# Performance work log

Measured on AMD Instinct MI355X. Metric: run time of the kernel, lower is better.

The kernel has to match this reference:

```python
import jax, jax.numpy as jnp
import numpy as np

N_NODES = 100000


def setup_inputs() -> dict:
    key = jax.random.key(0)
    k1, k2, k3 = jax.random.split(key, 3)
    x = jax.random.normal(k1, (N_NODES, 256), dtype=jnp.float32)
    edge_index = jax.random.randint(k2, (2, 1600000), 0, N_NODES, dtype=jnp.int64)
    W = jax.random.normal(k3, (256, 128), dtype=jnp.float32) * (1.0 / np.sqrt(256.0))
    b = jnp.zeros((128,), dtype=jnp.float32)
    alpha = jnp.full((128,), 0.25, dtype=jnp.float32)  # PReLU default init
    return {"x": x, "edge_index": edge_index, "W": W, "b": b, "alpha": alpha}


def reference(x, edge_index, W, b, alpha):
    N = x.shape[0]
    # --- GCNConv: add self-loops ---
    loops = jnp.arange(N, dtype=edge_index.dtype)
    row = jnp.concatenate([edge_index[0], loops])  # source nodes
    col = jnp.concatenate([edge_index[1], loops])  # destination nodes
    # symmetric normalization: deg computed at destinations (self-loops => deg >= 1)
    deg = jax.ops.segment_sum(jnp.ones(col.shape, x.dtype), col, num_segments=N)
    dinv = jax.lax.rsqrt(deg)
    norm = dinv[row] * dinv[col]  # [E+N]
    # linear transform then normalized scatter-add aggregation
    h = x @ W  # [N, H]
    msg = h[row] * norm[:, None]  # [E+N, H]
    out = jax.ops.segment_sum(msg, col, num_segments=N) + b  # bias after aggregation
    # --- PReLU (per-channel) ---
    return jnp.where(out >= 0, out, alpha * out)
```

## Files before the change

kernel.cpp:

```cpp
#include <hip/hip_runtime.h>

constexpr int KDIM  = 256;
constexpr int HDIM  = 128;
constexpr int BK    = 128;
constexpr int CHUNK = 8192;
constexpr int NBMAX = 800;

typedef __bf16 bf16x8 __attribute__((ext_vector_type(8)));
typedef float  f32x4  __attribute__((ext_vector_type(4)));

__device__ __forceinline__ ushort f2bf(float f) {
    unsigned u = __float_as_uint(f);
    unsigned r = (u + 0x7fffu + ((u >> 16) & 1u)) >> 16;
    return (ushort)r;
}

__device__ __forceinline__ void acc8i(float* a, uint2 u, float s) {
    int x = (int)u.x, y = (int)u.y;
    a[0] += s * (float)((x << 24) >> 24);
    a[1] += s * (float)((x << 16) >> 24);
    a[2] += s * (float)((x <<  8) >> 24);
    a[3] += s * (float)( x        >> 24);
    a[4] += s * (float)((y << 24) >> 24);
    a[5] += s * (float)((y << 16) >> 24);
    a[6] += s * (float)((y <<  8) >> 24);
    a[7] += s * (float)( y        >> 24);
}

__global__ __launch_bounds__(512) void prep_sort_kernel(
    const float* __restrict__ W, ushort* __restrict__ Wt, char* __restrict__ hsb8,
    float* __restrict__ hscale,
    const int* __restrict__ row, const int* __restrict__ col,
    uint* __restrict__ ebuf, int* __restrict__ histG, int* __restrict__ localOff,
    int n, int e, int nbv, int gblk) {
    __shared__ uint dst[CHUNK];
    __shared__ int hist[NBMAX], excl[NBMAX], cur[NBMAX];
    __shared__ int ws2[8];
    int b = blockIdx.x, t = threadIdx.x;
    if (b < 8) {
        int g = b * 512 + t;
        int lane = g & 63, cn = g >> 6;
        int c = cn >> 3, nf = cn & 7;
        int ncol = nf * 16 + (lane & 15);
        int k0 = c * 32 + (lane >> 4) * 8;
        ushort* dp = Wt + (size_t)g * 8;
        #pragma unroll
        for (int j = 0; j < 8; ++j) dp[j] = f2bf(W[(k0 + j) * HDIM + ncol]);
        return;
    }
    if (b == 8) {
        if (t < 32) ((uint*)(hsb8 + (size_t)n * HDIM))[t] = 0;
        if (t == 32) hscale[n] = 0.f;
        return;
    }
    int g = b - 9;
    int lane = t & 63, w = t >> 6;
    for (int i = t; i < nbv; i += 512) hist[i] = 0;
    __syncthreads();
    int lo = g * CHUNK, hi = min(lo + CHUNK, e);
    int colr[16];
    #pragma unroll
    for (int k = 0; k < 4; ++k) {
        int i0 = lo + (k * 512 + t) * 4;
        if (i0 + 3 < hi) {
            int4 c4 = *(const int4*)(col + i0);
            colr[k * 4 + 0] = c4.x; colr[k * 4 + 1] = c4.y;
            colr[k * 4 + 2] = c4.z; colr[k * 4 + 3] = c4.w;
            atomicAdd(&hist[c4.x >> 7], 1); atomicAdd(&hist[c4.y >> 7], 1);
            atomicAdd(&hist[c4.z >> 7], 1); atomicAdd(&hist[c4.w >> 7], 1);
        } else {
            #pragma unroll
            for (int j = 0; j < 4; ++j) {
                int i = i0 + j;
                int c = (i < hi) ? col[i] : -1;
                colr[k * 4 + j] = c;
                if (c >= 0) atomicAdd(&hist[c >> 7], 1);
            }
        }
    }
    __syncthreads();
    {
        int b0 = t * 2;
        int h0 = (b0 < nbv) ? hist[b0] : 0;
        int h1 = (b0 + 1 < nbv) ? hist[b0 + 1] : 0;
        int s = h0 + h1, incl = s;
        #pragma unroll
        for (int d = 1; d < 64; d <<= 1) { int u = __shfl_up(incl, d, 64); if (lane >= d) incl += u; }
        if (lane == 63) ws2[w] = incl;
        __syncthreads();
        int add = 0;
        #pragma unroll
        for (int i = 0; i < 8; ++i) if (i < w) add += ws2[i];
        int run = add + incl - s;
        if (b0 < nbv)     { excl[b0] = run;          cur[b0] = run; }
        if (b0 + 1 < nbv) { excl[b0 + 1] = run + h0; cur[b0 + 1] = run + h0; }
    }
    __syncthreads();
    #pragma unroll
    for (int k = 0; k < 4; ++k) {
        int i0 = lo + (k * 512 + t) * 4;
        if (i0 + 3 < hi) {
            int4 r4 = *(const int4*)(row + i0);
            int rr[4] = {r4.x, r4.y, r4.z, r4.w};
            #pragma unroll
            for (int j = 0; j < 4; ++j) {
                int c = colr[k * 4 + j];
                int p = atomicAdd(&cur[c >> 7], 1);
                dst[p] = ((uint)rr[j] << 7) | (uint)(c & 127);
            }
        } else {
            #pragma unroll
            for (int j = 0; j < 4; ++j) {
                int i = i0 + j, c = colr[k * 4 + j];
                if (c >= 0) {
                    int p = atomicAdd(&cur[c >> 7], 1);
                    dst[p] = ((uint)row[i] << 7) | (uint)(c & 127);
                }
            }
        }
    }
    __syncthreads();
    int cnt = hi - lo;
    for (int k = 0; k < 4; ++k) {
        int i0 = (k * 512 + t) * 4;
        if (i0 + 3 < cnt) *(uint4*)(ebuf + lo + i0) = *(uint4*)&dst[i0];
        else for (int j = 0; j < 4; ++j) if (i0 + j < cnt) ebuf[lo + i0 + j] = dst[i0 + j];
    }
    for (int i = t; i < nbv; i += 512) {
        histG[i * gblk + g]    = hist[i];
        localOff[i * gblk + g] = excl[i];
    }
}

__global__ __launch_bounds__(256) void scanA_kernel(const int* __restrict__ in,
                                                    int* __restrict__ partial, int n) {
    int t = threadIdx.x, base = blockIdx.x * 1024;
    int s = 0;
    #pragma unroll
    for (int j = 0; j < 4; ++j) {
        int i = base + j * 256 + t;
        if (i < n) s += in[i];
    }
    __shared__ int ws[4];
    #pragma unroll
    for (int d = 1; d < 64; d <<= 1) s += __shfl_xor(s, d, 64);
    int lane = t & 63, w = t >> 6;
    if (lane == 0) ws[w] = s;
    __syncthreads();
    if (t == 0) partial[blockIdx.x] = ws[0] + ws[1] + ws[2] + ws[3];
}

__global__ void scanB_kernel(int* __restrict__ partial, int nb) {
    int t = threadIdx.x;
    int v = (t < nb) ? partial[t] : 0;
    int orig = v;
    int lane = t & 63, w = t >> 6;
    #pragma unroll
    for (int d = 1; d < 64; d <<= 1) { int u = __shfl_up(v, d, 64); if (lane >= d) v += u; }
    __shared__ int ws[4];
    if (lane == 63) ws[w] = v;
    __syncthreads();
    int add = 0;
    #pragma unroll
    for (int i = 0; i < 4; ++i) if (i < w) add += ws[i];
    if (t < nb) partial[t] = v + add - orig;
}

__global__ __launch_bounds__(256) void scanC_kernel(const int* __restrict__ in,
                                                    const int* __restrict__ partial,
                                                    int* __restrict__ out, int n) {
    int t = threadIdx.x, base = blockIdx.x * 1024;
    int vals[4], tsum = 0;
    #pragma unroll
    for (int j = 0; j < 4; ++j) {
        int i = base + t * 4 + j;
        vals[j] = (i < n) ? in[i] : 0;
        tsum += vals[j];
    }
    int lane = t & 63, w = t >> 6;
    int incl = tsum;
    #pragma unroll
    for (int d = 1; d < 64; d <<= 1) { int u = __shfl_up(incl, d, 64); if (lane >= d) incl += u; }
    __shared__ int ws[4];
    if (lane == 63) ws[w] = incl;
    __syncthreads();
    int add = partial[blockIdx.x];
    #pragma unroll
    for (int i = 0; i < 4; ++i) if (i < w) add += ws[i];
    int run = add + incl - tsum;
    #pragma unroll
    for (int j = 0; j < 4; ++j) {
        int i = base + t * 4 + j;
        if (i < n) out[i] = run;
        run += vals[j];
    }
}

__global__ __launch_bounds__(256) void fine_kernel(const uint* __restrict__ ebuf,
                                                   const int* __restrict__ histG,
                                                   const int* __restrict__ localOff,
                                                   const int* __restrict__ histS,
                                                   uint* __restrict__ csr,
                                                   int* __restrict__ deg,
                                                   int* __restrict__ offs,
                                                   float* __restrict__ dinv,
                                                   int e, int nbv, int gblk, int n) {
    __shared__ uint elist[4096];
    __shared__ uint csrl[4096];
    __shared__ int hist[BK], excl[BK], cur[BK];
    int b = blockIdx.x, t = threadIdx.x;
    int seg0 = histS[b * gblk];
    int seg1 = (b + 1 < nbv) ? histS[(b + 1) * gblk] : e;
    int cnt = min(seg1 - seg0, 4096);

    if (t < BK) { hist[t] = 0; cur[t] = 0; }
    for (int g = t; g < gblk; g += 256) {
        int c   = histG[b * gblk + g];
        int src = g * CHUNK + localOff[b * gblk + g];
        int dst = histS[b * gblk + g] - seg0;
        for (int i = 0; i < c; ++i) elist[dst + i] = ebuf[src + i];
    }
    __syncthreads();
    for (int i = t; i < cnt; i += 256) atomicAdd(&hist[elist[i] & 127], 1);
    __syncthreads();
    if (t < 64) {
        int v0 = hist[2 * t], v1 = hist[2 * t + 1];
        int s = v0 + v1, incl = s;
        #pragma unroll
        for (int d = 1; d < 64; d <<= 1) { int u = __shfl_up(incl, d, 64); if (t >= d) incl += u; }
        int base = incl - s;
        excl[2 * t] = base; excl[2 * t + 1] = base + v0;
    }
    __syncthreads();
    for (int i = t; i < cnt; i += 256) {
        uint v = elist[i];
        int d = v & 127;
        int r = atomicAdd(&cur[d], 1);
        csrl[excl[d] + r] = v >> 7;
    }
    __syncthreads();
    for (int i = t; i < cnt; i += 256) csr[seg0 + i] = csrl[i];
    if (t < BK) {
        int node = b * BK + t;
        if (node < n) {
            int dg = hist[t];
            deg[node]  = dg;
            offs[node] = seg0 + excl[t];
            dinv[node] = rsqrtf((float)(dg + 1));
        }
    }
}


constexpr int MT = 64;
constexpr int XS_STRIDE = 264;

__global__ __launch_bounds__(256) void gemm_kernel(const float* __restrict__ x,
                                                   const ushort* __restrict__ Wt,
                                                   const float* __restrict__ dinv,
                                                   char* __restrict__ hsb8,
                                                   float* __restrict__ hscale, int n) {
    __shared__ ushort xs[MT * XS_STRIDE];
    __shared__ float sdinv[MT];
    __shared__ uint rmaxs[16];
    int t = threadIdx.x, lane = t & 63, w = t >> 6;
    int row0 = blockIdx.x * MT;

    bf16x8 bfrag[8][2];
    #pragma unroll
    for (int c = 0; c < 8; ++c)
        #pragma unroll
        for (int f = 0; f < 2; ++f)
            bfrag[c][f] = *(const bf16x8*)(Wt + (size_t)(((c * 8) + (w * 2 + f)) * 64 + lane) * 8);

    #pragma unroll
    for (int i = 0; i < 16; ++i) {
        int rl = w * 16 + i;
        int gr = row0 + rl; if (gr >= n) gr = n - 1;
        float4 v = *(const float4*)(x + (size_t)gr * KDIM + lane * 4);
        ushort4 o;
        o.x = f2bf(v.x); o.y = f2bf(v.y); o.z = f2bf(v.z); o.w = f2bf(v.w);
        *(ushort4*)(xs + rl * XS_STRIDE + lane * 4) = o;
    }
    if (t < MT) { int g = row0 + t; sdinv[t] = dinv[(g < n) ? g : (n - 1)]; }
    __syncthreads();

    for (int s = 0; s < MT / 16; ++s) {
        f32x4 acc0 = {0.f, 0.f, 0.f, 0.f}, acc1 = {0.f, 0.f, 0.f, 0.f};
        #pragma unroll
        for (int c = 0; c < 8; ++c) {
            const ushort* ap = xs + (s * 16 + (lane & 15)) * XS_STRIDE + c * 32 + (lane >> 4) * 8;
            bf16x8 afrag = *(const bf16x8*)ap;
            acc0 = __builtin_amdgcn_mfma_f32_16x16x32_bf16(afrag, bfrag[c][0], acc0, 0, 0, 0);
            acc1 = __builtin_amdgcn_mfma_f32_16x16x32_bf16(afrag, bfrag[c][1], acc1, 0, 0, 0);
        }
        if (t < 16) rmaxs[t] = 0;
        __syncthreads();
        float v0[4], v1[4];
        #pragma unroll
        for (int reg = 0; reg < 4; ++reg) {
            int rl = s * 16 + (lane >> 4) * 4 + reg;
            int gr = row0 + rl;
            if (gr < n) {
                float d = sdinv[rl];
                v0[reg] = acc0[reg] * d;
                v1[reg] = acc1[reg] * d;
                float m = fmaxf(fabsf(v0[reg]), fabsf(v1[reg]));
                atomicMax(&rmaxs[(lane >> 4) * 4 + reg], __float_as_uint(m));
            }
        }
        __syncthreads();
        #pragma unroll
        for (int reg = 0; reg < 4; ++reg) {
            int rl = s * 16 + (lane >> 4) * 4 + reg;
            int gr = row0 + rl;
            if (gr < n) {
                float rm = __uint_as_float(rmaxs[(lane >> 4) * 4 + reg]);
                float inv = (rm > 0.f) ? 127.f / rm : 0.f;
                int q0 = __float2int_rn(v0[reg] * inv);
                int q1 = __float2int_rn(v1[reg] * inv);
                int col0 = w * 32 + (lane & 15);
                hsb8[(size_t)gr * HDIM + col0]      = (char)q0;
                hsb8[(size_t)gr * HDIM + col0 + 16] = (char)q1;
            }
        }
        if (t < 16) {
            int gr = row0 + s * 16 + t;
            if (gr < n) hscale[gr] = __uint_as_float(rmaxs[t]) * (1.f / 127.f);
        }
        __syncthreads();
    }
}

__global__ __launch_bounds__(256) void aggregate_kernel(
    const char* __restrict__ hsb8, const float* __restrict__ hscale,
    const int* __restrict__ offs, const int* __restrict__ deg,
    const uint* __restrict__ csr, const float* __restrict__ dinv,
    const float* __restrict__ b, const float* __restrict__ alpha,
    float* __restrict__ out, int n) {
    int wv = threadIdx.x >> 6, lane = threadIdx.x & 63;
    int grp = lane >> 4, li = lane & 15;
    int node = blockIdx.x * 16 + wv * 4 + grp;
    bool valid = node < n;
    int nd   = valid ? node : n;
    int base = valid ? offs[node] : 0;
    int cnt  = valid ? deg[node] : 0;
    const uint2* hs2 = (const uint2*)hsb8;

    float a[8];
    #pragma unroll
    for (int i = 0; i < 8; ++i) a[i] = 0.f;

    uint2 su = hs2[(size_t)nd * 16 + li];
    acc8i(a, su, hscale[nd]);

    for (int it = 0; it < cnt; it += 16) {
        int src_l = (it + li < cnt) ? (int)__builtin_nontemporal_load(csr + base + it + li) : n;

        int sA[8];
        #pragma unroll
        for (int k = 0; k < 8; ++k) sA[k] = __shfl(src_l, grp * 16 + k, 64);
        uint2 uA[8];
        float scA[8];
        #pragma unroll
        for (int k = 0; k < 8; ++k) uA[k] = hs2[(size_t)sA[k] * 16 + li];
        #pragma unroll
        for (int k = 0; k < 8; ++k) scA[k] = hscale[sA[k]];
        #pragma unroll
        for (int k = 0; k < 8; ++k) acc8i(a, uA[k], scA[k]);

        if (it + 8 < cnt) {
            int sB[8];
            #pragma unroll
            for (int k = 0; k < 8; ++k) sB[k] = __shfl(src_l, grp * 16 + 8 + k, 64);
            uint2 uB[8];
            float scB[8];
            #pragma unroll
            for (int k = 0; k < 8; ++k) uB[k] = hs2[(size_t)sB[k] * 16 + li];
            #pragma unroll
            for (int k = 0; k < 8; ++k) scB[k] = hscale[sB[k]];
            #pragma unroll
            for (int k = 0; k < 8; ++k) acc8i(a, uB[k], scB[k]);
        }
    }

    if (valid) {
        float dc = dinv[node];
        int c0 = li * 8;
        float o[8];
        #pragma unroll
        for (int i = 0; i < 8; ++i) {
            float v = fmaf(dc, a[i], b[c0 + i]);
            o[i] = v >= 0.f ? v : alpha[c0 + i] * v;
        }
        float* op = out + (size_t)node * HDIM + c0;
        f32x4 v0 = {o[0], o[1], o[2], o[3]};
        f32x4 v1 = {o[4], o[5], o[6], o[7]};
        __builtin_nontemporal_store(v0, (f32x4*)op);
        __builtin_nontemporal_store(v1, (f32x4*)(op + 4));
    }
}


extern "C" void kernel_launch(void* const* d_in, const int* in_sizes, int n_in,
                              void* d_out, int out_size, void* d_ws, size_t ws_size,
                              hipStream_t stream) {
    const float* x     = (const float*)d_in[0];
    const int*   ei    = (const int*)d_in[1];
    const float* W     = (const float*)d_in[2];
    const float* b     = (const float*)d_in[3];
    const float* alpha = (const float*)d_in[4];
    float* out = (float*)d_out;

    int E = in_sizes[1] / 2;
    int N = in_sizes[0] / KDIM;
    int NB = (N + BK - 1) / BK;
    int GBLK = (E + CHUNK - 1) / CHUNK;
    int SCAN_N = NB * GBLK;

    char*  hsb8   = (char*)d_ws;
    float* hscale = (float*)(hsb8 + (size_t)(N + 1) * HDIM);
    ushort* Wt    = (ushort*)(hscale + (N + 1));
    float* dinv   = (float*)(Wt + 32768);
    int* deg      = (int*)(dinv + N);
    int* offs     = deg + N;
    int* histG    = offs + N;
    int* localOff = histG + SCAN_N;
    int* histS    = localOff + SCAN_N;
    int* partial  = histS + SCAN_N;
    uint* ebuf    = (uint*)(partial + 512);
    uint* csr     = ebuf + (size_t)GBLK * CHUNK;

    const int* rowp = ei;
    const int* colp = ei + E;

    int nbScan = (SCAN_N + 1023) / 1024;

    hipLaunchKernelGGL(prep_sort_kernel, dim3(9 + GBLK), dim3(512), 0, stream,
                       W, Wt, hsb8, hscale, rowp, colp, ebuf, histG, localOff, N, E, NB, GBLK);
    hipLaunchKernelGGL(scanA_kernel, dim3(nbScan), dim3(256), 0, stream, histG, partial, SCAN_N);
    hipLaunchKernelGGL(scanB_kernel, dim3(1), dim3(256), 0, stream, partial, nbScan);
    hipLaunchKernelGGL(scanC_kernel, dim3(nbScan), dim3(256), 0, stream, histG, partial, histS, SCAN_N);
    hipLaunchKernelGGL(fine_kernel, dim3(NB), dim3(256), 0, stream,
                       ebuf, histG, localOff, histS, csr, deg, offs, dinv, E, NB, GBLK, N);
    hipLaunchKernelGGL(gemm_kernel, dim3((N + MT - 1) / MT), dim3(256), 0, stream,
                       x, Wt, dinv, hsb8, hscale, N);
    hipLaunchKernelGGL(aggregate_kernel, dim3((N + 15) / 16), dim3(256), 0, stream,
                       hsb8, hscale, offs, deg, csr, dinv, b, alpha, out, N);
}
```

Baseline: 281.5 us.

## Fuse CSR construction into aggregation and fold degree scaling into row scales

Drops the three-pass global scan and the separate fine-sort kernel. Each 128-node aggregation block now rebuilds its local CSR in shared memory from the coarse-bucketed edge buffer, using an in-block prefix scan over chunk counts. The per-source degree normalization moves out of the GEMM into a small degscale kernel that multiplies the quantization scales, and the destination dinv is computed inline from the local histogram. This cuts launches and global traffic for the CSR, offs, deg and dinv arrays. In exchange, aggregation runs on far fewer blocks with heavy LDS use, which reduces parallelism for the latency-bound gathers, and the edge buffer is read twice.

```diff
diff --git a/kernel.cpp b/kernel.cpp
--- a/kernel.cpp
+++ b/kernel.cpp
@@ -132,136 +132,15 @@
     }
 }
 
-__global__ __launch_bounds__(256) void scanA_kernel(const int* __restrict__ in,
-                                                    int* __restrict__ partial, int n) {
-    int t = threadIdx.x, base = blockIdx.x * 1024;
-    int s = 0;
-    #pragma unroll
-    for (int j = 0; j < 4; ++j) {
-        int i = base + j * 256 + t;
-        if (i < n) s += in[i];
-    }
-    __shared__ int ws[4];
-    #pragma unroll
-    for (int d = 1; d < 64; d <<= 1) s += __shfl_xor(s, d, 64);
-    int lane = t & 63, w = t >> 6;
-    if (lane == 0) ws[w] = s;
-    __syncthreads();
-    if (t == 0) partial[blockIdx.x] = ws[0] + ws[1] + ws[2] + ws[3];
-}
-
-__global__ void scanB_kernel(int* __restrict__ partial, int nb) {
-    int t = threadIdx.x;
-    int v = (t < nb) ? partial[t] : 0;
-    int orig = v;
-    int lane = t & 63, w = t >> 6;
-    #pragma unroll
-    for (int d = 1; d < 64; d <<= 1) { int u = __shfl_up(v, d, 64); if (lane >= d) v += u; }
-    __shared__ int ws[4];
-    if (lane == 63) ws[w] = v;
-    __syncthreads();
-    int add = 0;
-    #pragma unroll
-    for (int i = 0; i < 4; ++i) if (i < w) add += ws[i];
-    if (t < nb) partial[t] = v + add - orig;
-}
-
-__global__ __launch_bounds__(256) void scanC_kernel(const int* __restrict__ in,
-                                                    const int* __restrict__ partial,
-                                                    int* __restrict__ out, int n) {
-    int t = threadIdx.x, base = blockIdx.x * 1024;
-    int vals[4], tsum = 0;
-    #pragma unroll
-    for (int j = 0; j < 4; ++j) {
-        int i = base + t * 4 + j;
-        vals[j] = (i < n) ? in[i] : 0;
-        tsum += vals[j];
-    }
-    int lane = t & 63, w = t >> 6;
-    int incl = tsum;
-    #pragma unroll
-    for (int d = 1; d < 64; d <<= 1) { int u = __shfl_up(incl, d, 64); if (lane >= d) incl += u; }
-    __shared__ int ws[4];
-    if (lane == 63) ws[w] = incl;
-    __syncthreads();
-    int add = partial[blockIdx.x];
-    #pragma unroll
-    for (int i = 0; i < 4; ++i) if (i < w) add += ws[i];
-    int run = add + incl - tsum;
-    #pragma unroll
-    for (int j = 0; j < 4; ++j) {
-        int i = base + t * 4 + j;
-        if (i < n) out[i] = run;
-        run += vals[j];
-    }
-}
-
-__global__ __launch_bounds__(256) void fine_kernel(const uint* __restrict__ ebuf,
-                                                   const int* __restrict__ histG,
-                                                   const int* __restrict__ localOff,
-                                                   const int* __restrict__ histS,
-                                                   uint* __restrict__ csr,
-                                                   int* __restrict__ deg,
-                                                   int* __restrict__ offs,
-                                                   float* __restrict__ dinv,
-                                                   int e, int nbv, int gblk, int n) {
-    __shared__ uint elist[4096];
-    __shared__ uint csrl[4096];
-    __shared__ int hist[BK], excl[BK], cur[BK];
-    int b = blockIdx.x, t = threadIdx.x;
-    int seg0 = histS[b * gblk];
-    int seg1 = (b + 1 < nbv) ? histS[(b + 1) * gblk] : e;
-    int cnt = min(seg1 - seg0, 4096);
-
-    if (t < BK) { hist[t] = 0; cur[t] = 0; }
-    for (int g = t; g < gblk; g += 256) {
-        int c   = histG[b * gblk + g];
-        int src = g * CHUNK + localOff[b * gblk + g];
-        int dst = histS[b * gblk + g] - seg0;
-        for (int i = 0; i < c; ++i) elist[dst + i] = ebuf[src + i];
-    }
-    __syncthreads();
-    for (int i = t; i < cnt; i += 256) atomicAdd(&hist[elist[i] & 127], 1);
-    __syncthreads();
-    if (t < 64) {
-        int v0 = hist[2 * t], v1 = hist[2 * t + 1];
-        int s = v0 + v1, incl = s;
-        #pragma unroll
-        for (int d = 1; d < 64; d <<= 1) { int u = __shfl_up(incl, d, 64); if (t >= d) incl += u; }
-        int base = incl - s;
-        excl[2 * t] = base; excl[2 * t + 1] = base + v0;
-    }
-    __syncthreads();
-    for (int i = t; i < cnt; i += 256) {
-        uint v = elist[i];
-        int d = v & 127;
-        int r = atomicAdd(&cur[d], 1);
-        csrl[excl[d] + r] = v >> 7;
-    }
-    __syncthreads();
-    for (int i = t; i < cnt; i += 256) csr[seg0 + i] = csrl[i];
-    if (t < BK) {
-        int node = b * BK + t;
-        if (node < n) {
-            int dg = hist[t];
-            deg[node]  = dg;
-            offs[node] = seg0 + excl[t];
-            dinv[node] = rsqrtf((float)(dg + 1));
-        }
-    }
-}
-
 
 constexpr int MT = 64;
 constexpr int XS_STRIDE = 264;
 
 __global__ __launch_bounds__(256) void gemm_kernel(const float* __restrict__ x,
                                                    const ushort* __restrict__ Wt,
-                                                   const float* __restrict__ dinv,
                                                    char* __restrict__ hsb8,
                                                    float* __restrict__ hscale, int n) {
     __shared__ ushort xs[MT * XS_STRIDE];
-    __shared__ float sdinv[MT];
     __shared__ uint rmaxs[16];
     int t = threadIdx.x, lane = t & 63, w = t >> 6;
     int row0 = blockIdx.x * MT;
@@ -282,7 +161,6 @@
         o.x = f2bf(v.x); o.y = f2bf(v.y); o.z = f2bf(v.z); o.w = f2bf(v.w);
         *(ushort4*)(xs + rl * XS_STRIDE + lane * 4) = o;
     }
-    if (t < MT) { int g = row0 + t; sdinv[t] = dinv[(g < n) ? g : (n - 1)]; }
     __syncthreads();
 
     for (int s = 0; s < MT / 16; ++s) {
@@ -296,16 +174,12 @@
         }
         if (t < 16) rmaxs[t] = 0;
         __syncthreads();
-        float v0[4], v1[4];
         #pragma unroll
         for (int reg = 0; reg < 4; ++reg) {
             int rl = s * 16 + (lane >> 4) * 4 + reg;
             int gr = row0 + rl;
             if (gr < n) {
-                float d = sdinv[rl];
-                v0[reg] = acc0[reg] * d;
-                v1[reg] = acc1[reg] * d;
-                float m = fmaxf(fabsf(v0[reg]), fabsf(v1[reg]));
+                float m = fmaxf(fabsf(acc0[reg]), fabsf(acc1[reg]));
                 atomicMax(&rmaxs[(lane >> 4) * 4 + reg], __float_as_uint(m));
             }
         }
@@ -317,8 +191,8 @@
             if (gr < n) {
                 float rm = __uint_as_float(rmaxs[(lane >> 4) * 4 + reg]);
                 float inv = (rm > 0.f) ? 127.f / rm : 0.f;
-                int q0 = __float2int_rn(v0[reg] * inv);
-                int q1 = __float2int_rn(v1[reg] * inv);
+                int q0 = __float2int_rn(acc0[reg] * inv);
+                int q1 = __float2int_rn(acc1[reg] * inv);
                 int col0 = w * 32 + (lane & 15);
                 hsb8[(size_t)gr * HDIM + col0]      = (char)q0;
                 hsb8[(size_t)gr * HDIM + col0 + 16] = (char)q1;
@@ -332,72 +206,121 @@
     }
 }
 
-__global__ __launch_bounds__(256) void aggregate_kernel(
+__global__ __launch_bounds__(256) void degscale_kernel(
+    const uint* __restrict__ ebuf, const int* __restrict__ histG,
+    const int* __restrict__ localOff, float* __restrict__ hscale,
+    int n, int gblk) {
+    __shared__ int hist[BK];
+    int b = blockIdx.x, t = threadIdx.x;
+    if (t < BK) hist[t] = 0;
+    __syncthreads();
+    int grp = t >> 4, li = t & 15;
+    for (int g = grp; g < gblk; g += 16) {
+        int c   = histG[b * gblk + g];
+        int src = g * CHUNK + localOff[b * gblk + g];
+        for (int i = li; i < c; i += 16) atomicAdd(&hist[ebuf[src + i] & 127], 1);
+    }
+    __syncthreads();
+    if (t < BK) {
+        int node = b * BK + t;
+        if (node < n) hscale[node] *= rsqrtf((float)(hist[t] + 1));
+    }
+}
+
+__global__ __launch_bounds__(256) void agg_kernel(
     const char* __restrict__ hsb8, const float* __restrict__ hscale,
-    const int* __restrict__ offs, const int* __restrict__ deg,
-    const uint* __restrict__ csr, const float* __restrict__ dinv,
-    const float* __restrict__ b, const float* __restrict__ alpha,
-    float* __restrict__ out, int n) {
-    int wv = threadIdx.x >> 6, lane = threadIdx.x & 63;
-    int grp = lane >> 4, li = lane & 15;
-    int node = blockIdx.x * 16 + wv * 4 + grp;
-    bool valid = node < n;
-    int nd   = valid ? node : n;
-    int base = valid ? offs[node] : 0;
-    int cnt  = valid ? deg[node] : 0;
+    const uint* __restrict__ ebuf, const int* __restrict__ histG,
+    const int* __restrict__ localOff, const float* __restrict__ bias,
+    const float* __restrict__ alpha, float* __restrict__ out, int n, int gblk) {
+    __shared__ uint elist[4096];
+    __shared__ uint csrl[4096];
+    __shared__ int hist[BK], excl[BK], cur[BK];
+    __shared__ int segOff[256];
+    int b = blockIdx.x, t = threadIdx.x;
+
+    segOff[t] = (t < gblk) ? histG[b * gblk + t] : 0;
+    if (t < BK) { hist[t] = 0; cur[t] = 0; }
+    __syncthreads();
+    for (int d = 1; d < 256; d <<= 1) {
+        int v = (t >= d) ? segOff[t - d] : 0;
+        __syncthreads();
+        segOff[t] += v;
+        __syncthreads();
+    }
+    int cnt = min(segOff[255], 4096);
+    int grp = t >> 4, li = t & 15;
+    for (int g = grp; g < gblk; g += 16) {
+        int pre = (g == 0) ? 0 : min(segOff[g - 1], 4096);
+        int end = min(segOff[g], 4096);
+        int c   = end - pre;
+        int src = g * CHUNK + localOff[b * gblk + g];
+        for (int i = li; i < c; i += 16) elist[pre + i] = ebuf[src + i];
+    }
+    __syncthreads();
+    for (int i = t; i < cnt; i += 256) atomicAdd(&hist[elist[i] & 127], 1);
+    __syncthreads();
+    if (t < 64) {
+        int v0 = hist[2 * t], v1 = hist[2 * t + 1];
+        int s = v0 + v1, incl = s;
+        #pragma unroll
+        for (int d = 1; d < 64; d <<= 1) { int u = __shfl_up(incl, d, 64); if (t >= d) incl += u; }
+        int base = incl - s;
+        excl[2 * t] = base; excl[2 * t + 1] = base + v0;
+    }
+    __syncthreads();
+    for (int i = t; i < cnt; i += 256) {
+        uint v = elist[i];
+        int d = v & 127;
+        int r = atomicAdd(&cur[d], 1);
+        csrl[excl[d] + r] = v >> 7;
+    }
+    __syncthreads();
+
     const uint2* hs2 = (const uint2*)hsb8;
-
-    float a[8];
-    #pragma unroll
-    for (int i = 0; i < 8; ++i) a[i] = 0.f;
-
-    uint2 su = hs2[(size_t)nd * 16 + li];
-    acc8i(a, su, hscale[nd]);
-
-    for (int it = 0; it < cnt; it += 16) {
-        int src_l = (it + li < cnt) ? (int)__builtin_nontemporal_load(csr + base + it + li) : n;
-
-        int sA[8];
-        #pragma unroll
-        for (int k = 0; k < 8; ++k) sA[k] = __shfl(src_l, grp * 16 + k, 64);
-        uint2 uA[8];
-        float scA[8];
-        #pragma unroll
-        for (int k = 0; k < 8; ++k) uA[k] = hs2[(size_t)sA[k] * 16 + li];
-        #pragma unroll
-        for (int k = 0; k < 8; ++k) scA[k] = hscale[sA[k]];
-        #pragma unroll
-        for (int k = 0; k < 8; ++k) acc8i(a, uA[k], scA[k]);
-
-        if (it + 8 < cnt) {
-            int sB[8];
-            #pragma unroll
-            for (int k = 0; k < 8; ++k) sB[k] = __shfl(src_l, grp * 16 + 8 + k, 64);
-            uint2 uB[8];
-            float scB[8];
-            #pragma unroll
-            for (int k = 0; k < 8; ++k) uB[k] = hs2[(size_t)sB[k] * 16 + li];
-            #pragma unroll
-            for (int k = 0; k < 8; ++k) scB[k] = hscale[sB[k]];
-            #pragma unroll
-            for (int k = 0; k < 8; ++k) acc8i(a, uB[k], scB[k]);
-        }
-    }
-
-    if (valid) {
-        float dc = dinv[node];
-        int c0 = li * 8;
-        float o[8];
-        #pragma unroll
-        for (int i = 0; i < 8; ++i) {
-            float v = fmaf(dc, a[i], b[c0 + i]);
-            o[i] = v >= 0.f ? v : alpha[c0 + i] * v;
-        }
-        float* op = out + (size_t)node * HDIM + c0;
-        f32x4 v0 = {o[0], o[1], o[2], o[3]};
-        f32x4 v1 = {o[4], o[5], o[6], o[7]};
-        __builtin_nontemporal_store(v0, (f32x4*)op);
-        __builtin_nontemporal_store(v1, (f32x4*)(op + 4));
+    for (int nl = grp; nl < BK; nl += 16) {
+        int node = b * BK + nl;
+        bool valid = node < n;
+        int nd   = valid ? node : n;
+        int base = excl[nl];
+        int c    = hist[nl];
+
+        float a[8];
+        #pragma unroll
+        for (int i = 0; i < 8; ++i) a[i] = 0.f;
+
+        uint2 su = hs2[(size_t)nd * 16 + li];
+        acc8i(a, su, hscale[nd]);
+
+        for (int it = 0; it < c; it += 8) {
+            int s[8];
+            #pragma unroll
+            for (int k = 0; k < 8; ++k)
+                s[k] = (it + k < c) ? (int)csrl[base + it + k] : n;
+            uint2 u[8];
+            float sc[8];
+            #pragma unroll
+            for (int k = 0; k < 8; ++k) u[k] = hs2[(size_t)s[k] * 16 + li];
+            #pragma unroll
+            for (int k = 0; k < 8; ++k) sc[k] = hscale[s[k]];
+            #pragma unroll
+            for (int k = 0; k < 8; ++k) acc8i(a, u[k], sc[k]);
+        }
+
+        if (valid) {
+            float dc = rsqrtf((float)(c + 1));
+            int c0 = li * 8;
+            float o[8];
+            #pragma unroll
+            for (int i = 0; i < 8; ++i) {
+                float v = fmaf(dc, a[i], bias[c0 + i]);
+                o[i] = v >= 0.f ? v : alpha[c0 + i] * v;
+            }
+            float* op = out + (size_t)node * HDIM + c0;
+            f32x4 v0 = {o[0], o[1], o[2], o[3]};
+            f32x4 v1 = {o[4], o[5], o[6], o[7]};
+            __builtin_nontemporal_store(v0, (f32x4*)op);
+            __builtin_nontemporal_store(v1, (f32x4*)(op + 4));
+        }
     }
 }
 
@@ -421,30 +344,19 @@
     char*  hsb8   = (char*)d_ws;
     float* hscale = (float*)(hsb8 + (size_t)(N + 1) * HDIM);
     ushort* Wt    = (ushort*)(hscale + (N + 1));
-    float* dinv   = (float*)(Wt + 32768);
-    int* deg      = (int*)(dinv + N);
-    int* offs     = deg + N;
-    int* histG    = offs + N;
+    int* histG    = (int*)(Wt + 32768);
     int* localOff = histG + SCAN_N;
-    int* histS    = localOff + SCAN_N;
-    int* partial  = histS + SCAN_N;
-    uint* ebuf    = (uint*)(partial + 512);
-    uint* csr     = ebuf + (size_t)GBLK * CHUNK;
+    uint* ebuf    = (uint*)(localOff + SCAN_N);
 
     const int* rowp = ei;
     const int* colp = ei + E;
 
-    int nbScan = (SCAN_N + 1023) / 1024;
-
     hipLaunchKernelGGL(prep_sort_kernel, dim3(9 + GBLK), dim3(512), 0, stream,
                        W, Wt, hsb8, hscale, rowp, colp, ebuf, histG, localOff, N, E, NB, GBLK);
-    hipLaunchKernelGGL(scanA_kernel, dim3(nbScan), dim3(256), 0, stream, histG, partial, SCAN_N);
-    hipLaunchKernelGGL(scanB_kernel, dim3(1), dim3(256), 0, stream, partial, nbScan);
-    hipLaunchKernelGGL(scanC_kernel, dim3(nbScan), dim3(256), 0, stream, histG, partial, histS, SCAN_N);
-    hipLaunchKernelGGL(fine_kernel, dim3(NB), dim3(256), 0, stream,
-                       ebuf, histG, localOff, histS, csr, deg, offs, dinv, E, NB, GBLK, N);
     hipLaunchKernelGGL(gemm_kernel, dim3((N + MT - 1) / MT), dim3(256), 0, stream,
-                       x, Wt, dinv, hsb8, hscale, N);
-    hipLaunchKernelGGL(aggregate_kernel, dim3((N + 15) / 16), dim3(256), 0, stream,
-                       hsb8, hscale, offs, deg, csr, dinv, b, alpha, out, N);
-}
+                       x, Wt, hsb8, hscale, N);
+    hipLaunchKernelGGL(degscale_kernel, dim3(NB), dim3(256), 0, stream,
+                       ebuf, histG, localOff, hscale, N, GBLK);
+    hipLaunchKernelGGL(agg_kernel, dim3(NB), dim3(256), 0, stream,
+                       hsb8, hscale, ebuf, histG, localOff, b, alpha, out, N, GBLK);
+}
```

Result: slower. 294.6 us (+4.7%).
